# Kernel tuning notes

Measured on AMD Instinct MI355X. Metric: run time of the kernel, lower is better.

Reference implementation:

```python
import jax, jax.numpy as jnp
import numpy as np

KEY_DIM = 32
VALUE_DIM = 64
HEADS = 8
CHAN = 256


def conv1x1(x, w, b):
    # x: [b, c, h, w], w: [out, c], b: [out]  (1x1 conv == channel matmul)
    return jnp.einsum('bchw,oc->bohw', x, w) + b[None, :, None, None]


def setup_inputs() -> dict:
    key = jax.random.key(0)
    ks = jax.random.split(key, 9)
    b, c, h, w = 8, CHAN, 128, 128
    qk_dim = KEY_DIM * HEADS   # 256
    v_dim = VALUE_DIM * HEADS  # 512
    s = 0.02
    return {
        'x':  jax.random.normal(ks[0], (b, c, h, w), jnp.float32),
        'Wq': jax.random.normal(ks[1], (qk_dim, c), jnp.float32) * s,
        'bq': jnp.zeros((qk_dim,), jnp.float32),
        'Wk': jax.random.normal(ks[2], (qk_dim, c), jnp.float32) * s,
        'bk': jnp.zeros((qk_dim,), jnp.float32),
        'Wv': jax.random.normal(ks[3], (v_dim, c), jnp.float32) * s,
        'bv': jnp.zeros((v_dim,), jnp.float32),
        'Wo': jax.random.normal(ks[4], (c, v_dim), jnp.float32) * s,
        'bo': jnp.zeros((c,), jnp.float32),
    }


def reference(x, Wq, bq, Wk, bk, Wv, bv, Wo, bo):
    b, c, h, w = x.shape
    n = h * w
    scale = KEY_DIM ** (-0.25)
    # 1x1 conv projections, reshape to [b, heads, d, n]
    q = conv1x1(x, Wq, bq).reshape(b, HEADS, KEY_DIM, n) * scale
    k = conv1x1(x, Wk, bk).reshape(b, HEADS, KEY_DIM, n) * scale
    v = conv1x1(x, Wv, bv).reshape(b, HEADS, VALUE_DIM, n)
    # softmax over sequence positions for keys
    k = jax.nn.softmax(k, axis=-1)
    # norm_queries=True: softmax over key dim for queries
    q = jax.nn.softmax(q, axis=-2)
    # linear attention: context [b,h,d_k,d_v], then output [b,h,d_v,n]
    ctx = jnp.einsum('bhdn,bhen->bhde', k, v)
    out = jnp.einsum('bhdn,bhde->bhen', q, ctx)
    out = out.reshape(b, HEADS * VALUE_DIM, h, w)
    return conv1x1(out, Wo, bo)
```

## Files before the change

### kernel.cpp

```cpp
#include <hip/hip_runtime.h>
#include <hip/hip_bf16.h>
#include <cstddef>


constexpr int   NPIX     = 16384;
constexpr float QK_SCALE = 0.42044820762685725f;

typedef __attribute__((ext_vector_type(8))) short          bf16x8;
typedef __attribute__((ext_vector_type(8))) unsigned short u16x8;
typedef __attribute__((ext_vector_type(4))) float          f32x4;

__device__ __forceinline__ float bf2f(unsigned short v) {
    union { unsigned int u; float f; } c; c.u = ((unsigned int)v) << 16; return c.f;
}
__device__ __forceinline__ unsigned short f2bf(float f) {
    union { __hip_bfloat16 h; unsigned short s; } c; c.h = __float2bfloat16(f); return c.s;
}
__device__ __forceinline__ void gload_lds16(const void* g, void* l) {
    __builtin_amdgcn_global_load_lds(
        (const __attribute__((address_space(1))) unsigned int*)g,
        (__attribute__((address_space(3))) unsigned int*)l, 16, 0, 0);
}

typedef unsigned short lds_row32[32];

__global__ __launch_bounds__(256) void prep(
    const float* __restrict__ Wq, const float* __restrict__ Wk,
    unsigned short* __restrict__ Wqb, unsigned short* __restrict__ Wkb)
{
    const int i = blockIdx.x * 256 + threadIdx.x;
    Wqb[i] = f2bf(Wq[i]);
    Wkb[i] = f2bf(Wk[i]);
}

template<bool QPASS>
__global__ __launch_bounds__(256) void proj_mfma(
    const float* __restrict__ x, const unsigned short* __restrict__ Wb,
    const float* __restrict__ bias, unsigned short* __restrict__ eout,
    float* __restrict__ ksump2)
{
    __shared__ alignas(16) unsigned char smem[36864];
    lds_row32* As1 = (lds_row32*)smem;
    unsigned short (*BsT)[40] = (unsigned short(*)[40])(smem + 16384);
    const int b  = blockIdx.z;
    const int m0 = blockIdx.y * 128;
    const int n0 = blockIdx.x * 128;
    const int t  = threadIdx.x;
    const int w  = t >> 6, l = t & 63;
    const int lm = l & 15, lg = l >> 4;
    const int mwl = (w & 1) * 64;
    const int nwl = (w >> 1) * 64;
    const int lgs = (lg ^ ((lm & 3) ^ ((lm >> 2) & 3))) * 8;
    const int r16 = l >> 2;
    const int scb = ((l & 3) ^ ((r16 & 3) ^ ((r16 >> 2) & 3))) * 8;

    const unsigned short* Abase = Wb + (size_t)m0 * 256;
    const float* xb = x + (size_t)b * 256 * NPIX + n0;
    const int np = (t & 63) * 2, kq = (t >> 6) * 8;

    f32x4 acc[4][4] = {};
    for (int k0 = 0; k0 < 256; k0 += 32) {
        #pragma unroll
        for (int i = 0; i < 2; ++i) {
            const int row0 = w*32 + i*16;
            gload_lds16(Abase + (size_t)(row0 + r16)*256 + k0 + scb, &As1[row0][0]);
        }
        {
            const float* src = xb + (size_t)(k0 + kq) * NPIX + np;
            float2 v[8];
            #pragma unroll
            for (int r = 0; r < 8; ++r)
                v[r] = *(const float2*)(src + (size_t)r * NPIX);
            u16x8 pa, pb;
            #pragma unroll
            for (int r = 0; r < 8; ++r) { pa[r] = f2bf(v[r].x); pb[r] = f2bf(v[r].y); }
            *(u16x8*)&BsT[np][kq]     = pa;
            *(u16x8*)&BsT[np + 1][kq] = pb;
        }
        __syncthreads();
        bf16x8 afr[4], bfr[4];
        #pragma unroll
        for (int i = 0; i < 4; ++i)
            afr[i] = *(const bf16x8*)&As1[mwl + i*16 + lm][lgs];
        #pragma unroll
        for (int j = 0; j < 4; ++j)
            bfr[j] = *(const bf16x8*)&BsT[nwl + j*16 + lm][lg*8];
        #pragma unroll
        for (int i = 0; i < 4; ++i)
            #pragma unroll
            for (int j = 0; j < 4; ++j)
                acc[i][j] = __builtin_amdgcn_mfma_f32_16x16x32_bf16(afr[i], bfr[j], acc[i][j], 0, 0, 0);
        __syncthreads();
    }

    unsigned short (*Cs)[64][72] = (unsigned short(*)[64][72])smem;
    const int mw = m0 + mwl, nw = n0 + nwl;
    float ksloc[4][4];
    #pragma unroll
    for (int i = 0; i < 4; ++i) {
        const f32x4 bb4 = *(const f32x4*)(bias + mw + i*16 + lg*4);
        #pragma unroll
        for (int r = 0; r < 4; ++r) {
            const int row = i*16 + lg*4 + r;
            float cs = 0.f;
            #pragma unroll
            for (int j = 0; j < 4; ++j) {
                const int col = j*16 + lm;
                const unsigned short bs = f2bf(__expf(QK_SCALE * (acc[i][j][r] + bb4[r])));
                if (QPASS) Cs[w][col][row] = bs;
                else { Cs[w][row][col] = bs; cs += bf2f(bs); }
            }
            ksloc[i][r] = cs;
        }
    }
    if (!QPASS) {
        #pragma unroll
        for (int i = 0; i < 4; ++i)
            #pragma unroll
            for (int r = 0; r < 4; ++r) {
                float v = ksloc[i][r];
                v += __shfl_xor(v, 1, 64);
                v += __shfl_xor(v, 2, 64);
                v += __shfl_xor(v, 4, 64);
                v += __shfl_xor(v, 8, 64);
                if (lm == 0) {
                    const int nt2 = blockIdx.x * 2 + (w >> 1);
                    ksump2[((size_t)b*256 + nt2)*256 + mw + i*16 + lg*4 + r] = v;
                }
            }
    }
    __syncthreads();

    if (QPASS) {
        unsigned short* dst = eout + ((size_t)b * NPIX + nw + l) * 256 + mw;
        u16x8 vv[8];
        float z0 = 0.f, z1 = 0.f;
        #pragma unroll
        for (int s8 = 0; s8 < 8; ++s8) {
            vv[s8] = *(const u16x8*)&Cs[w][l][s8*8];
            float ps = 0.f;
            #pragma unroll
            for (int u = 0; u < 8; ++u) ps += bf2f(vv[s8][u]);
            if (s8 < 4) z0 += ps; else z1 += ps;
        }
        const float iz0 = 1.0f / z0, iz1 = 1.0f / z1;
        #pragma unroll
        for (int s8 = 0; s8 < 8; ++s8) {
            const float iz = (s8 < 4) ? iz0 : iz1;
            u16x8 o;
            #pragma unroll
            for (int u = 0; u < 8; ++u) o[u] = f2bf(bf2f(vv[s8][u]) * iz);
            *(u16x8*)(dst + s8*8) = o;
        }
    } else {
        unsigned short* dst = eout + ((size_t)b * 256 + mw + l) * NPIX + nw;
        #pragma unroll
        for (int s8 = 0; s8 < 8; ++s8)
            *(u16x8*)(dst + s8*8) = *(const u16x8*)&Cs[w][l][s8*8];
    }
}

__global__ __launch_bounds__(256) void ksum_red(
    const float* __restrict__ ksump2, float* __restrict__ ksum)
{
    const int t = threadIdx.x;
    const int row = blockIdx.x * 32 + (t >> 3);
    const int b = row >> 8, c = row & 255;
    const int nt0 = t & 7;
    float s = 0.f;
    #pragma unroll 8
    for (int i = 0; i < 32; ++i)
        s += ksump2[((size_t)b*256 + nt0 + 8*i)*256 + c];
    s += __shfl_xor(s, 1, 64);
    s += __shfl_xor(s, 2, 64);
    s += __shfl_xor(s, 4, 64);
    if (nt0 == 0) ksum[row] = s;
}

template<int NCH>
__global__ __launch_bounds__(256) void t_mfma(
    const unsigned short* __restrict__ ek, const float* __restrict__ x,
    float* __restrict__ Tpart)
{
    __shared__ alignas(16) unsigned char smem[32768];
    lds_row32* As = (lds_row32*)smem;
    lds_row32* Bs = (lds_row32*)(smem + 16384);
    const int bid  = blockIdx.x;
    const int v    = bid & 7, s = bid >> 3;
    const int gidx = s >> 2, q = s & 3;
    const int group = v + 8 * gidx;
    const int b = group / NCH, chunk = group % NCH;
    const int mt = (q >> 1) * 128, ct = (q & 1) * 128;
    constexpr int CHPX = NPIX / NCH;

    const int t = threadIdx.x;
    const int w = t >> 6, l = t & 63;
    const int lm = l & 15, lg = l >> 4;
    const int mw = (w & 1) * 64, cw = (w >> 1) * 64;
    const int r16 = l >> 2;
    const int scb = ((l & 3) ^ ((r16 & 3) ^ ((r16 >> 2) & 3))) * 8;
    const int lgs = (lg ^ ((lm & 3) ^ ((lm >> 2) & 3))) * 8;
    const int brq = t >> 3;
    const int bc4 = (t & 7) * 4;
    const int bslot = (t & 7) >> 1;
    const int bhalf = (t & 1) * 4;

    const unsigned short* Abase = ek + ((size_t)b*256 + mt) * NPIX;
    const float*          Bbase = x  + ((size_t)b*256 + ct) * NPIX;
    const int p0base = chunk * CHPX;

    f32x4 breg[4];
    f32x4 acc[4][4] = {};

    #pragma unroll
    for (int i = 0; i < 2; ++i) {
        const int row0 = w*32 + i*16;
        gload_lds16(Abase + (size_t)(row0 + r16) * NPIX + p0base + scb, &As[row0][0]);
    }
    #pragma unroll
    for (int it = 0; it < 4; ++it)
        breg[it] = *(const f32x4*)(Bbase + (size_t)(it*32 + brq) * NPIX + p0base + bc4);
    #pragma unroll
    for (int it = 0; it < 4; ++it) {
        const int row = it*32 + brq;
        const int sl = bslot ^ ((row & 3) ^ ((row >> 2) & 3));
        unsigned short o[4] = { f2bf(breg[it].x), f2bf(breg[it].y),
                                f2bf(breg[it].z), f2bf(breg[it].w) };
        *(ushort4*)&Bs[row][sl*8 + bhalf] = *(ushort4*)o;
    }
    __syncthreads();

    constexpr int ITERS = CHPX / 32;
    for (int t8 = 0; t8 < ITERS; ++t8) {
        const int cur = t8 & 1;
        if (t8 < ITERS - 1) {
            const int p0 = p0base + (t8 + 1) * 32;
            #pragma unroll
            for (int i = 0; i < 2; ++i) {
                const int row0 = w*32 + i*16;
                gload_lds16(Abase + (size_t)(row0 + r16) * NPIX + p0 + scb,
                            &As[(cur^1)*128 + row0][0]);
            }
            #pragma unroll
            for (int it = 0; it < 4; ++it)
                breg[it] = *(const f32x4*)(Bbase + (size_t)(it*32 + brq) * NPIX + p0 + bc4);
        }
        bf16x8 afr[4], bfr[4];
        #pragma unroll
        for (int i = 0; i < 4; ++i)
            afr[i] = *(const bf16x8*)&As[cur*128 + mw + i*16 + lm][lgs];
        #pragma unroll
        for (int j = 0; j < 4; ++j)
            bfr[j] = *(const bf16x8*)&Bs[cur*128 + cw + j*16 + lm][lgs];
        #pragma unroll
        for (int i = 0; i < 4; ++i)
            #pragma unroll
            for (int j = 0; j < 4; ++j)
                acc[i][j] = __builtin_amdgcn_mfma_f32_16x16x32_bf16(afr[i], bfr[j], acc[i][j], 0, 0, 0);
        if (t8 < ITERS - 1) {
            #pragma unroll
            for (int it = 0; it < 4; ++it) {
                const int row = it*32 + brq;
                const int sl = bslot ^ ((row & 3) ^ ((row >> 2) & 3));
                unsigned short o[4] = { f2bf(breg[it].x), f2bf(breg[it].y),
                                        f2bf(breg[it].z), f2bf(breg[it].w) };
                *(ushort4*)&Bs[(cur^1)*128 + row][sl*8 + bhalf] = *(ushort4*)o;
            }
        }
        __syncthreads();
    }

    float* dst = Tpart + ((size_t)(b*NCH + chunk) * 256) * 256;
    #pragma unroll
    for (int i = 0; i < 4; ++i)
        #pragma unroll
        for (int r = 0; r < 4; ++r) {
            const int gm = mt + mw + i*16 + lg*4 + r;
            #pragma unroll
            for (int j = 0; j < 4; ++j)
                dst[(size_t)gm * 256 + ct + cw + j*16 + lm] = acc[i][j][r];
        }
}

template<int NCH>
__global__ __launch_bounds__(256) void treduce(
    float* __restrict__ Tpart, const float* __restrict__ ksum)
{
    const int gid = blockIdx.x * 256 + threadIdx.x;
    const int b   = gid >> 14;
    const int rem = gid & 16383;
    const int r   = rem >> 6;
    const int c4  = (rem & 63) * 4;
    float* base = Tpart + (((size_t)b*NCH) * 256 + r) * 256 + c4;
    f32x4 s = *(f32x4*)base;
    #pragma unroll
    for (int ch = 1; ch < NCH; ++ch) {
        f32x4 v = *(const f32x4*)(base + (size_t)ch * 65536);
        s.x += v.x; s.y += v.y; s.z += v.z; s.w += v.w;
    }
    const float inv = 1.0f / ksum[b*256 + r];
    s.x *= inv; s.y *= inv; s.z *= inv; s.w *= inv;
    *(f32x4*)base = s;
}

template<int NCH>
__global__ __launch_bounds__(256) void ctx_pass(
    const float* __restrict__ Tpart, const float* __restrict__ Wv,
    const float* __restrict__ bv, float* __restrict__ ctx)
{
    const int gid = blockIdx.x * 256 + threadIdx.x;
    const int b   = gid >> 14;
    const int rem = gid & 16383;
    const int h   = rem >> 11;
    const int de  = rem & 2047;
    const int d   = de >> 6;
    const int e   = de & 63;
    const float* tp = Tpart + (((size_t)b*NCH) * 256 + h*32 + d) * 256;
    const float* wv = Wv + (size_t)(h*64 + e) * 256;
    float sx = 0.f, sy = 0.f, sz = 0.f, sw = 0.f;
    #pragma unroll 8
    for (int c = 0; c < 256; c += 4) {
        f32x4 a = *(const f32x4*)(tp + c);
        f32x4 wv4 = *(const f32x4*)(wv + c);
        sx = fmaf(a.x, wv4.x, sx); sy = fmaf(a.y, wv4.y, sy);
        sz = fmaf(a.z, wv4.z, sz); sw = fmaf(a.w, wv4.w, sw);
    }
    ctx[gid] = (sx + sy) + (sz + sw) + bv[h*64 + e];
}

__global__ __launch_bounds__(256) void mpass(
    const float* __restrict__ ctx, const float* __restrict__ Wo,
    unsigned short* __restrict__ Mb)
{
    const int gid = blockIdx.x * 256 + threadIdx.x;
    const int b   = gid >> 16;
    const int rem = gid & 65535;
    const int o   = rem >> 8;
    const int dg  = rem & 255;
    const int h   = dg >> 5;
    const float* cp = ctx + ((size_t)b*8 + h) * 2048 + (dg & 31) * 64;
    const float* wp = Wo + (size_t)o * 512 + h*64;
    float sx = 0.f, sy = 0.f, sz = 0.f, sw = 0.f;
    #pragma unroll
    for (int e = 0; e < 64; e += 4) {
        f32x4 a = *(const f32x4*)(cp + e);
        f32x4 wv = *(const f32x4*)(wp + e);
        sx = fmaf(a.x, wv.x, sx); sy = fmaf(a.y, wv.y, sy);
        sz = fmaf(a.z, wv.z, sz); sw = fmaf(a.w, wv.w, sw);
    }
    Mb[((size_t)b*256 + o) * 256 + dg] = f2bf((sx + sy) + (sz + sw));
}

__global__ __launch_bounds__(256) void out_mfma(
    const unsigned short* __restrict__ eqT, const unsigned short* __restrict__ Mb,
    const float* __restrict__ bo, float* __restrict__ out)
{
    __shared__ alignas(16) unsigned char smem[32768];
    lds_row32* As0 = (lds_row32*)smem;
    lds_row32* Bs0 = (lds_row32*)(smem + 16384);
    const int b  = blockIdx.z;
    const int m0 = blockIdx.y * 128;
    const int n0 = blockIdx.x * 128;
    const int t  = threadIdx.x;
    const int w  = t >> 6, l = t & 63;
    const int lm = l & 15, lg = l >> 4;
    const int mwl = (w & 1) * 64, nwl = (w >> 1) * 64;
    const int lgs = (lg ^ ((lm & 3) ^ ((lm >> 2) & 3))) * 8;
    const int r16 = l >> 2;
    const int scb = ((l & 3) ^ ((r16 & 3) ^ ((r16 >> 2) & 3))) * 8;

    const unsigned short* Abase = Mb  + ((size_t)b*256 + m0) * 256;
    const unsigned short* Bbase = eqT + ((size_t)b*NPIX + n0) * 256;

    auto stage = [&](int buf, int k0) {
        #pragma unroll
        for (int i = 0; i < 2; ++i) {
            const int row0 = w*32 + i*16;
            gload_lds16(Abase + (size_t)(row0 + r16)*256 + k0 + scb, &As0[buf*128 + row0][0]);
            gload_lds16(Bbase + (size_t)(row0 + r16)*256 + k0 + scb, &Bs0[buf*128 + row0][0]);
        }
    };

    f32x4 acc[4][4] = {};
    stage(0, 0);
    __syncthreads();
    for (int t8 = 0; t8 < 8; ++t8) {
        const int cur = t8 & 1;
        if (t8 < 7) stage(cur ^ 1, (t8 + 1) * 32);
        bf16x8 afr[4], bfr[4];
        #pragma unroll
        for (int i = 0; i < 4; ++i)
            afr[i] = *(const bf16x8*)&As0[cur*128 + mwl + i*16 + lm][lgs];
        #pragma unroll
        for (int j = 0; j < 4; ++j)
            bfr[j] = *(const bf16x8*)&Bs0[cur*128 + nwl + j*16 + lm][lgs];
        #pragma unroll
        for (int i = 0; i < 4; ++i)
            #pragma unroll
            for (int j = 0; j < 4; ++j)
                acc[i][j] = __builtin_amdgcn_mfma_f32_16x16x32_bf16(afr[i], bfr[j], acc[i][j], 0, 0, 0);
        __syncthreads();
    }

    #pragma unroll
    for (int i = 0; i < 4; ++i) {
        const f32x4 bb4 = *(const f32x4*)(bo + m0 + mwl + i*16 + lg*4);
        #pragma unroll
        for (int r = 0; r < 4; ++r) {
            const int gm = m0 + mwl + i*16 + lg*4 + r;
            float* dst = out + ((size_t)b*256 + gm) * NPIX + n0 + nwl;
            #pragma unroll
            for (int j = 0; j < 4; ++j)
                dst[j*16 + lm] = acc[i][j][r] + bb4[r];
        }
    }
}

extern "C" void kernel_launch(void* const* d_in, const int* in_sizes, int n_in,
                              void* d_out, int out_size, void* d_ws, size_t ws_size,
                              hipStream_t stream)
{
    const float* x  = (const float*)d_in[0];
    const float* Wq = (const float*)d_in[1];
    const float* bq = (const float*)d_in[2];
    const float* Wk = (const float*)d_in[3];
    const float* bk = (const float*)d_in[4];
    const float* Wv = (const float*)d_in[5];
    const float* bv = (const float*)d_in[6];
    const float* Wo = (const float*)d_in[7];
    const float* bo = (const float*)d_in[8];
    float* out = (float*)d_out;
    char* wsb = (char*)d_ws;

    const bool big = ws_size >= (size_t)102506496;
    if (!big && ws_size < (size_t)89399296) return;

    unsigned short* ekq = (unsigned short*)wsb;
    float *Tpart, *ksump2, *ksum, *ctx;
    unsigned short *Mb, *Wqb, *Wkb;
    if (big) {
        Tpart  = (float*)(wsb + 67108864);
        ksump2 = (float*)(wsb + 67108864);
        ctx    = (float*)(wsb + 100663296);
        ksum   = (float*)(wsb + 101187584);
        Mb     = (unsigned short*)(wsb + 101195776);
        Wqb    = (unsigned short*)(wsb + 102244352);
        Wkb    = (unsigned short*)(wsb + 102375424);
    } else {
        Tpart  = (float*)(wsb + 67108864);
        ksump2 = (float*)(wsb + 67108864);
        ctx    = (float*)(wsb + 83886080);
        ksum   = (float*)(wsb + 84410368);
        Mb     = (unsigned short*)(wsb + 88088576);
        Wqb    = (unsigned short*)(wsb + 89137152);
        Wkb    = (unsigned short*)(wsb + 89268224);
    }

    prep            <<<256,             256, 0, stream>>>(Wq, Wk, Wqb, Wkb);
    proj_mfma<false><<<dim3(128, 2, 8), 256, 0, stream>>>(x, Wkb, bk, ekq, ksump2);
    ksum_red        <<<64,              256, 0, stream>>>(ksump2, ksum);
    if (big) {
        t_mfma<16> <<<512, 256, 0, stream>>>(ekq, x, Tpart);
        treduce<16><<<512, 256, 0, stream>>>(Tpart, ksum);
        ctx_pass<16><<<512, 256, 0, stream>>>(Tpart, Wv, bv, ctx);
    } else {
        t_mfma<8>  <<<256, 256, 0, stream>>>(ekq, x, Tpart);
        treduce<8> <<<512, 256, 0, stream>>>(Tpart, ksum);
        ctx_pass<8><<<512, 256, 0, stream>>>(Tpart, Wv, bv, ctx);
    }
    mpass           <<<2048,            256, 0, stream>>>(ctx, Wo, Mb);
    proj_mfma<true> <<<dim3(128, 2, 8), 256, 0, stream>>>(x, Wqb, bq, ekq, ksump2);
    out_mfma        <<<dim3(128, 2, 8), 256, 0, stream>>>(ekq, Mb, bo, out);
}
```

Measured before the change: 253.3 us.

## Halve proj_mfma LDS via two-phase epilogue staging and raise occupancy

The projection kernel's shared memory shrinks from 36 KB to 18 KB. The epilogue staging buffer is now shared by the two wave halves in two phases with extra barriers, and launch bounds request 5 blocks per CU. The aim is higher occupancy so global loads and MFMA work can overlap better, at the cost of a serialised epilogue and possible register pressure. The small-workspace NCH=8 path is also dropped, and the kernels are no longer templated on NCH.

```diff
diff --git a/kernel.cpp b/kernel.cpp
--- a/kernel.cpp
+++ b/kernel.cpp
@@ -5,6 +5,7 @@
 
 constexpr int   NPIX     = 16384;
 constexpr float QK_SCALE = 0.42044820762685725f;
+constexpr int   NCH      = 16;
 
 typedef __attribute__((ext_vector_type(8))) short          bf16x8;
 typedef __attribute__((ext_vector_type(8))) unsigned short u16x8;
@@ -34,14 +35,14 @@
 }
 
 template<bool QPASS>
-__global__ __launch_bounds__(256) void proj_mfma(
+__global__ __launch_bounds__(256, 5) void proj_mfma(
     const float* __restrict__ x, const unsigned short* __restrict__ Wb,
     const float* __restrict__ bias, unsigned short* __restrict__ eout,
     float* __restrict__ ksump2)
 {
-    __shared__ alignas(16) unsigned char smem[36864];
+    __shared__ alignas(16) unsigned char smem[18432];
     lds_row32* As1 = (lds_row32*)smem;
-    unsigned short (*BsT)[40] = (unsigned short(*)[40])(smem + 16384);
+    unsigned short (*BsT)[40] = (unsigned short(*)[40])(smem + 8192);
     const int b  = blockIdx.z;
     const int m0 = blockIdx.y * 128;
     const int n0 = blockIdx.x * 128;
@@ -95,68 +96,78 @@
 
     unsigned short (*Cs)[64][72] = (unsigned short(*)[64][72])smem;
     const int mw = m0 + mwl, nw = n0 + nwl;
-    float ksloc[4][4];
-    #pragma unroll
-    for (int i = 0; i < 4; ++i) {
-        const f32x4 bb4 = *(const f32x4*)(bias + mw + i*16 + lg*4);
-        #pragma unroll
-        for (int r = 0; r < 4; ++r) {
-            const int row = i*16 + lg*4 + r;
-            float cs = 0.f;
-            #pragma unroll
-            for (int j = 0; j < 4; ++j) {
-                const int col = j*16 + lm;
-                const unsigned short bs = f2bf(__expf(QK_SCALE * (acc[i][j][r] + bb4[r])));
-                if (QPASS) Cs[w][col][row] = bs;
-                else { Cs[w][row][col] = bs; cs += bf2f(bs); }
-            }
-            ksloc[i][r] = cs;
-        }
-    }
-    if (!QPASS) {
-        #pragma unroll
-        for (int i = 0; i < 4; ++i)
-            #pragma unroll
-            for (int r = 0; r < 4; ++r) {
-                float v = ksloc[i][r];
-                v += __shfl_xor(v, 1, 64);
-                v += __shfl_xor(v, 2, 64);
-                v += __shfl_xor(v, 4, 64);
-                v += __shfl_xor(v, 8, 64);
-                if (lm == 0) {
-                    const int nt2 = blockIdx.x * 2 + (w >> 1);
-                    ksump2[((size_t)b*256 + nt2)*256 + mw + i*16 + lg*4 + r] = v;
+    const int cw = w & 1;
+    const int ph = w >> 1;
+
+    #pragma unroll
+    for (int phase = 0; phase < 2; ++phase) {
+        if (ph == phase) {
+            float ksloc[4][4];
+            #pragma unroll
+            for (int i = 0; i < 4; ++i) {
+                const f32x4 bb4 = *(const f32x4*)(bias + mw + i*16 + lg*4);
+                #pragma unroll
+                for (int r = 0; r < 4; ++r) {
+                    const int row = i*16 + lg*4 + r;
+                    float cs = 0.f;
+                    #pragma unroll
+                    for (int j = 0; j < 4; ++j) {
+                        const int col = j*16 + lm;
+                        const unsigned short bs = f2bf(__expf(QK_SCALE * (acc[i][j][r] + bb4[r])));
+                        if (QPASS) Cs[cw][col][row] = bs;
+                        else { Cs[cw][row][col] = bs; cs += bf2f(bs); }
+                    }
+                    ksloc[i][r] = cs;
                 }
             }
-    }
-    __syncthreads();
-
-    if (QPASS) {
-        unsigned short* dst = eout + ((size_t)b * NPIX + nw + l) * 256 + mw;
-        u16x8 vv[8];
-        float z0 = 0.f, z1 = 0.f;
-        #pragma unroll
-        for (int s8 = 0; s8 < 8; ++s8) {
-            vv[s8] = *(const u16x8*)&Cs[w][l][s8*8];
-            float ps = 0.f;
-            #pragma unroll
-            for (int u = 0; u < 8; ++u) ps += bf2f(vv[s8][u]);
-            if (s8 < 4) z0 += ps; else z1 += ps;
-        }
-        const float iz0 = 1.0f / z0, iz1 = 1.0f / z1;
-        #pragma unroll
-        for (int s8 = 0; s8 < 8; ++s8) {
-            const float iz = (s8 < 4) ? iz0 : iz1;
-            u16x8 o;
-            #pragma unroll
-            for (int u = 0; u < 8; ++u) o[u] = f2bf(bf2f(vv[s8][u]) * iz);
-            *(u16x8*)(dst + s8*8) = o;
-        }
-    } else {
-        unsigned short* dst = eout + ((size_t)b * 256 + mw + l) * NPIX + nw;
-        #pragma unroll
-        for (int s8 = 0; s8 < 8; ++s8)
-            *(u16x8*)(dst + s8*8) = *(const u16x8*)&Cs[w][l][s8*8];
+            if (!QPASS) {
+                #pragma unroll
+                for (int i = 0; i < 4; ++i)
+                    #pragma unroll
+                    for (int r = 0; r < 4; ++r) {
+                        float v = ksloc[i][r];
+                        v += __shfl_xor(v, 1, 64);
+                        v += __shfl_xor(v, 2, 64);
+                        v += __shfl_xor(v, 4, 64);
+                        v += __shfl_xor(v, 8, 64);
+                        if (lm == 0) {
+                            const int nt2 = blockIdx.x * 2 + (w >> 1);
+                            ksump2[((size_t)b*256 + nt2)*256 + mw + i*16 + lg*4 + r] = v;
+                        }
+                    }
+            }
+        }
+        __syncthreads();
+        if (ph == phase) {
+            if (QPASS) {
+                unsigned short* dst = eout + ((size_t)b * NPIX + nw + l) * 256 + mw;
+                u16x8 vv[8];
+                float z0 = 0.f, z1 = 0.f;
+                #pragma unroll
+                for (int s8 = 0; s8 < 8; ++s8) {
+                    vv[s8] = *(const u16x8*)&Cs[cw][l][s8*8];
+                    float ps = 0.f;
+                    #pragma unroll
+                    for (int u = 0; u < 8; ++u) ps += bf2f(vv[s8][u]);
+                    if (s8 < 4) z0 += ps; else z1 += ps;
+                }
+                const float iz0 = 1.0f / z0, iz1 = 1.0f / z1;
+                #pragma unroll
+                for (int s8 = 0; s8 < 8; ++s8) {
+                    const float iz = (s8 < 4) ? iz0 : iz1;
+                    u16x8 o;
+                    #pragma unroll
+                    for (int u = 0; u < 8; ++u) o[u] = f2bf(bf2f(vv[s8][u]) * iz);
+                    *(u16x8*)(dst + s8*8) = o;
+                }
+            } else {
+                unsigned short* dst = eout + ((size_t)b * 256 + mw + l) * NPIX + nw;
+                #pragma unroll
+                for (int s8 = 0; s8 < 8; ++s8)
+                    *(u16x8*)(dst + s8*8) = *(const u16x8*)&Cs[cw][l][s8*8];
+            }
+        }
+        __syncthreads();
     }
 }
 
@@ -177,7 +188,6 @@
     if (nt0 == 0) ksum[row] = s;
 }
 
-template<int NCH>
 __global__ __launch_bounds__(256) void t_mfma(
     const unsigned short* __restrict__ ek, const float* __restrict__ x,
     float* __restrict__ Tpart)
@@ -282,7 +292,6 @@
         }
 }
 
-template<int NCH>
 __global__ __launch_bounds__(256) void treduce(
     float* __restrict__ Tpart, const float* __restrict__ ksum)
 {
@@ -303,7 +312,6 @@
     *(f32x4*)base = s;
 }
 
-template<int NCH>
 __global__ __launch_bounds__(256) void ctx_pass(
     const float* __restrict__ Tpart, const float* __restrict__ Wv,
     const float* __restrict__ bv, float* __restrict__ ctx)
@@ -432,42 +440,23 @@
     float* out = (float*)d_out;
     char* wsb = (char*)d_ws;
 
-    const bool big = ws_size >= (size_t)102506496;
-    if (!big && ws_size < (size_t)89399296) return;
-
-    unsigned short* ekq = (unsigned short*)wsb;
-    float *Tpart, *ksump2, *ksum, *ctx;
-    unsigned short *Mb, *Wqb, *Wkb;
-    if (big) {
-        Tpart  = (float*)(wsb + 67108864);
-        ksump2 = (float*)(wsb + 67108864);
-        ctx    = (float*)(wsb + 100663296);
-        ksum   = (float*)(wsb + 101187584);
-        Mb     = (unsigned short*)(wsb + 101195776);
-        Wqb    = (unsigned short*)(wsb + 102244352);
-        Wkb    = (unsigned short*)(wsb + 102375424);
-    } else {
-        Tpart  = (float*)(wsb + 67108864);
-        ksump2 = (float*)(wsb + 67108864);
-        ctx    = (float*)(wsb + 83886080);
-        ksum   = (float*)(wsb + 84410368);
-        Mb     = (unsigned short*)(wsb + 88088576);
-        Wqb    = (unsigned short*)(wsb + 89137152);
-        Wkb    = (unsigned short*)(wsb + 89268224);
-    }
+    if (ws_size < (size_t)102506496) return;
+
+    unsigned short* ekq   = (unsigned short*)wsb;
+    float*          Tpart = (float*)(wsb + 67108864);
+    float*          ksump2= (float*)(wsb + 67108864);
+    float*          ctx   = (float*)(wsb + 100663296);
+    float*          ksum  = (float*)(wsb + 101187584);
+    unsigned short* Mb    = (unsigned short*)(wsb + 101195776);
+    unsigned short* Wqb   = (unsigned short*)(wsb + 102244352);
+    unsigned short* Wkb   = (unsigned short*)(wsb + 102375424);
 
     prep            <<<256,             256, 0, stream>>>(Wq, Wk, Wqb, Wkb);
     proj_mfma<false><<<dim3(128, 2, 8), 256, 0, stream>>>(x, Wkb, bk, ekq, ksump2);
     ksum_red        <<<64,              256, 0, stream>>>(ksump2, ksum);
-    if (big) {
-        t_mfma<16> <<<512, 256, 0, stream>>>(ekq, x, Tpart);
-        treduce<16><<<512, 256, 0, stream>>>(Tpart, ksum);
-        ctx_pass<16><<<512, 256, 0, stream>>>(Tpart, Wv, bv, ctx);
-    } else {
-        t_mfma<8>  <<<256, 256, 0, stream>>>(ekq, x, Tpart);
-        treduce<8> <<<512, 256, 0, stream>>>(Tpart, ksum);
-        ctx_pass<8><<<512, 256, 0, stream>>>(Tpart, Wv, bv, ctx);
-    }
+    t_mfma          <<<512,             256, 0, stream>>>(ekq, x, Tpart);
+    treduce         <<<512,             256, 0, stream>>>(Tpart, ksum);
+    ctx_pass        <<<512,             256, 0, stream>>>(Tpart, Wv, bv, ctx);
     mpass           <<<2048,            256, 0, stream>>>(ctx, Wo, Mb);
     proj_mfma<true> <<<dim3(128, 2, 8), 256, 0, stream>>>(x, Wqb, bq, ekq, ksump2);
     out_mfma        <<<dim3(128, 2, 8), 256, 0, stream>>>(ekq, Mb, bo, out);
```

New measurement: 407.7 us. 1.61x slower.
